# Kernel optimization log

Measured on AMD Instinct MI355X. Metric: run time of the kernel, lower is better.

## Reference

```python
import jax, jax.numpy as jnp
import numpy as np

B, S, D, H = 1, 4096, 768, 12
HID = 3072
HD = D // H  # 64
EPS = 1e-5


def _layer_norm(x, w, b):
    mean = jnp.mean(x, axis=-1, keepdims=True)
    var = jnp.mean(jnp.square(x - mean), axis=-1, keepdims=True)  # unbiased=False
    return w * ((x - mean) / jnp.sqrt(var + EPS)) + b


def setup_inputs() -> dict:
    key = jax.random.key(0)
    ks = jax.random.split(key, 8)
    s_d = 1.0 / np.sqrt(D)
    s_h = 1.0 / np.sqrt(HID)
    return {
        "x": jax.random.normal(ks[0], (B, S, D), dtype=jnp.float32),
        "Wqkv": jax.random.normal(ks[1], (D, 3 * D), dtype=jnp.float32) * s_d,
        "bqkv": jnp.zeros((3 * D,), dtype=jnp.float32),
        "Wo": jax.random.normal(ks[2], (D, D), dtype=jnp.float32) * s_d,
        "bo": jnp.zeros((D,), dtype=jnp.float32),
        "ln1_w": jnp.ones((D,), dtype=jnp.float32),
        "ln1_b": jnp.zeros((D,), dtype=jnp.float32),
        "W1": jax.random.normal(ks[3], (D, HID), dtype=jnp.float32) * s_d,
        "b1": jnp.zeros((HID,), dtype=jnp.float32),
        "W2": jax.random.normal(ks[4], (HID, D), dtype=jnp.float32) * s_h,
        "b2": jnp.zeros((D,), dtype=jnp.float32),
        "ln2_w": jnp.ones((D,), dtype=jnp.float32),
        "ln2_b": jnp.zeros((D,), dtype=jnp.float32),
    }


def reference(x, Wqkv, bqkv, Wo, bo, ln1_w, ln1_b, W1, b1, W2, b2, ln2_w, ln2_b):
    b, s, d = x.shape
    # --- multi-head self-attention (naive: full [B,H,S,S] scores) ---
    qkv = x @ Wqkv + bqkv                              # [B,S,3D]
    q, k, v = jnp.split(qkv, 3, axis=-1)
    split = lambda t: t.reshape(b, s, H, HD).transpose(0, 2, 1, 3)  # [B,H,S,hd]
    q, k, v = split(q), split(k), split(v)
    scores = jnp.einsum("bhqd,bhkd->bhqk", q, k) / jnp.sqrt(jnp.float32(HD))
    attn_w = jax.nn.softmax(scores, axis=-1)           # [B,H,S,S]
    h = jnp.einsum("bhqk,bhkd->bhqd", attn_w, v)
    h = h.transpose(0, 2, 1, 3).reshape(b, s, d)       # merge heads
    attn_out = h @ Wo + bo
    # --- post-norm residual 1 ---
    x1 = _layer_norm(x + attn_out, ln1_w, ln1_b)
    # --- FFN ---
    ff = jax.nn.gelu(x1 @ W1 + b1, approximate=False) @ W2 + b2
    # --- post-norm residual 2 ---
    return _layer_norm(x1 + ff, ln2_w, ln2_b)
```

## Files before the change

kernel.cpp:

```cpp
#include <hip/hip_runtime.h>
#include <hip/hip_bf16.h>

typedef __attribute__((ext_vector_type(8))) short bf16x8;
typedef __attribute__((ext_vector_type(4))) short short4v;
typedef __attribute__((ext_vector_type(4))) float f32x4;
typedef __attribute__((ext_vector_type(16))) float f32x16;
typedef __attribute__((ext_vector_type(4))) unsigned int uint4v;

__device__ inline unsigned short f2b(float f){
  unsigned int u = __float_as_uint(f);
  unsigned int r = (u + 0x7fffu + ((u >> 16) & 1u)) >> 16;
  return (unsigned short)r;
}
__device__ inline float b2f(unsigned short u){
  return __uint_as_float(((unsigned int)u) << 16);
}
__device__ inline unsigned int pk_fast(float lo, float hi){
  return ((__float_as_uint(hi) + 0x8000u) & 0xffff0000u)
       | ((__float_as_uint(lo) + 0x8000u) >> 16);
}
__device__ inline float pair_sum(float x){
  return x + __shfl_xor(x, 32);
}

__global__ __launch_bounds__(256) void prep_kernel(
    const float* __restrict__ Wqkv, short* __restrict__ WqkvT,
    const float* __restrict__ Wo,   short* __restrict__ WoT,
    const float* __restrict__ W1,   short* __restrict__ W1T,
    const float* __restrict__ W2,   short* __restrict__ W2T,
    const float* __restrict__ x,    short* __restrict__ xb){
  __shared__ float tile[32][33];
  const int b = blockIdx.x;
  const float* A; short* AT; int R, C, bx, by;
  if (b < 1728){ A=Wqkv; AT=WqkvT; R=768;  C=2304; bx=b%72;        by=b/72; }
  else if (b < 2304){ int c=b-1728; A=Wo; AT=WoT; R=768;  C=768;  bx=c%24; by=c/24; }
  else if (b < 4608){ int c=b-2304; A=W1; AT=W1T; R=768;  C=3072; bx=c%96; by=c/96; }
  else if (b < 6912){ int c=b-4608; A=W2; AT=W2T; R=3072; C=768;  bx=c%24; by=c/24; }
  else {
    int i = (b - 6912)*256 + threadIdx.x;
    float4 v = reinterpret_cast<const float4*>(x)[i];
    short4v o;
    o[0] = (short)f2b(v.x); o[1] = (short)f2b(v.y);
    o[2] = (short)f2b(v.z); o[3] = (short)f2b(v.w);
    reinterpret_cast<short4v*>(xb)[i] = o;
    return;
  }
  const int tx = threadIdx.x & 31, ty = threadIdx.x >> 5;
  const int c0 = bx*32, r0 = by*32;
  #pragma unroll
  for (int i = 0; i < 4; i++)
    tile[ty + i*8][tx] = A[(size_t)(r0 + ty + i*8)*C + c0 + tx];
  __syncthreads();
  #pragma unroll
  for (int i = 0; i < 4; i++){
    int c = c0 + ty + i*8, r = r0 + tx;
    AT[(size_t)c*R + r] = (short)f2b(tile[tx][ty + i*8]);
  }
}

template<int OUTMODE, int RESID, int GELU>
__global__ __launch_bounds__(256) void gemm_kernel(
    const short* __restrict__ A, const short* __restrict__ BT,
    const float* __restrict__ bias, const float* __restrict__ resid,
    float* __restrict__ outF, short* __restrict__ outB, short* __restrict__ outB2,
    short* __restrict__ outB3,
    int M, int N, int K)
{
  __shared__ short As[2][128*32];
  __shared__ short Bs[2][128*32];
  const int nwg = gridDim.x;
  const int wg = (blockIdx.x & 7) * (nwg >> 3) + (blockIdx.x >> 3);
  const int gx = N >> 7;
  const int bx = wg % gx, by = wg / gx;
  const int m0 = by * 128, n0 = bx * 128;

  const int lane = threadIdx.x & 63, wid = threadIdx.x >> 6;
  const int l15 = lane & 15, l4 = lane >> 4;
  const int wr = wid >> 1, wc = wid & 1;

  f32x4 acc[4][4];
  #pragma unroll
  for (int i = 0; i < 4; i++)
    #pragma unroll
    for (int j = 0; j < 4; j++) acc[i][j] = (f32x4){0.f,0.f,0.f,0.f};

  const int arow = wid*16 + (lane >> 2);
  const int sswz = (((lane & 3) ^ ((lane >> 3) & 3))) * 8;
  const short* Ag = A  + (size_t)(m0 + arow)*K + sswz;
  const short* Bg = BT + (size_t)(n0 + arow)*K + sswz;

  const int NT = K >> 5;

  auto STAGE = [&](int buf, int k0){
    #pragma unroll
    for (int p = 0; p < 2; p++){
      __builtin_amdgcn_global_load_lds(
          (const __attribute__((address_space(1))) void*)(Ag + (size_t)p*64*K + k0),
          (__attribute__((address_space(3))) void*)(&As[buf][(p*64 + wid*16)*32]), 16, 0, 0);
      __builtin_amdgcn_global_load_lds(
          (const __attribute__((address_space(1))) void*)(Bg + (size_t)p*64*K + k0),
          (__attribute__((address_space(3))) void*)(&Bs[buf][(p*64 + wid*16)*32]), 16, 0, 0);
    }
  };

  STAGE(0, 0);
  __syncthreads();

  const int rchunk = (l15 >> 1) & 3;
  for (int t = 0; t < NT; t++){
    if (t + 1 < NT) STAGE((t + 1) & 1, (t + 1) << 5);
    const short* as = &As[t & 1][0];
    const short* bs = &Bs[t & 1][0];
    bf16x8 av[4], bv[4];
    #pragma unroll
    for (int i = 0; i < 4; i++)
      av[i] = *(const bf16x8*)(as + (wr*64 + i*16 + l15)*32 + ((l4 ^ rchunk) * 8));
    #pragma unroll
    for (int i = 0; i < 4; i++)
      bv[i] = *(const bf16x8*)(bs + (wc*64 + i*16 + l15)*32 + ((l4 ^ rchunk) * 8));
    #pragma unroll
    for (int i = 0; i < 4; i++)
      #pragma unroll
      for (int j = 0; j < 4; j++)
        acc[i][j] = __builtin_amdgcn_mfma_f32_16x16x32_bf16(av[i], bv[j], acc[i][j], 0, 0, 0);
    __syncthreads();
  }

  if constexpr (OUTMODE == 2){
    #pragma unroll
    for (int i = 0; i < 4; i++){
      const int row0 = m0 + wr*64 + i*16 + l4*4;
      const size_t rQK = (size_t)(row0>>5)*2048 + (size_t)(row0&31)*8;
      const size_t rV  = (size_t)(row0>>5)*2048 + (size_t)((row0>>4)&1)*1024
                       + (size_t)((row0>>3)&1)*256 + (size_t)(row0&7);
      #pragma unroll
      for (int j = 0; j < 4; j++){
        const int col = n0 + wc*64 + j*16 + l15;
        const float bval = bias[col];
        const float v0 = acc[i][j][0] + bval, v1 = acc[i][j][1] + bval;
        const float v2 = acc[i][j][2] + bval, v3 = acc[i][j][3] + bval;
        if (col < 1536){
          const int c2 = (col < 768) ? col : (col - 768);
          short* dst = (col < 768) ? outB : outB2;
          const int head = c2 >> 6, dh = c2 & 63;
          const size_t base = (size_t)head*262144 + (size_t)(dh>>4)*512
                            + (size_t)((dh>>3)&1)*256 + (size_t)(dh&7) + rQK;
          dst[base]      = (short)f2b(v0);
          dst[base + 8]  = (short)f2b(v1);
          dst[base + 16] = (short)f2b(v2);
          dst[base + 24] = (short)f2b(v3);
        } else {
          const int c2 = col - 1536;
          const int head = c2 >> 6, dh = c2 & 63;
          const size_t base = (size_t)head*262144 + (size_t)(dh>>5)*512
                            + (size_t)(dh&31)*8 + rV;
          short4v sv;
          sv[0] = (short)f2b(v0); sv[1] = (short)f2b(v1);
          sv[2] = (short)f2b(v2); sv[3] = (short)f2b(v3);
          *(short4v*)(outB3 + base) = sv;
        }
      }
    }
  } else {
    #pragma unroll
    for (int i = 0; i < 4; i++){
      const int row0 = m0 + wr*64 + i*16 + l4*4;
      #pragma unroll
      for (int j = 0; j < 4; j++){
        const int col = n0 + wc*64 + j*16 + l15;
        const float bval = bias[col];
        #pragma unroll
        for (int jj = 0; jj < 4; jj++){
          const int row = row0 + jj;
          float v = acc[i][j][jj] + bval;
          if constexpr (RESID) v += resid[(size_t)row*N + col];
          if constexpr (GELU)  v = 0.5f * v * (1.f + erff(v * 0.70710678118654752f));
          if constexpr (OUTMODE == 0){
            outF[(size_t)row*N + col] = v;
          } else {
            outB[(size_t)row*N + col] = (short)f2b(v);
          }
        }
      }
    }
  }
}

__global__ __launch_bounds__(256) void attn5_kernel(
    const short* __restrict__ Qf, const short* __restrict__ Kf,
    const short* __restrict__ Vf, short* __restrict__ hout){
  __shared__ float Ols[4][32][33];
  __shared__ float Lls[4][32];
  const int head = blockIdx.y;
  const int qt = blockIdx.x;
  const int lane = threadIdx.x & 63, w = threadIdx.x >> 6;
  const int l31 = lane & 31, hi = lane >> 5;

  bf16x8 qf0, qf1, qf2, qf3;
  {
    const short* qp = Qf + (size_t)(head*128 + qt)*2048 + lane*8;
    const float SC = 0.125f * 1.44269504088896341f;
    bf16x8 tq[4];
    #pragma unroll
    for (int kd = 0; kd < 4; kd++){
      bf16x8 t = *(const bf16x8*)(qp + kd*512);
      #pragma unroll
      for (int i = 0; i < 8; i++)
        t[i] = (short)f2b(b2f((unsigned short)t[i]) * SC);
      tq[kd] = t;
    }
    qf0 = tq[0]; qf1 = tq[1]; qf2 = tq[2]; qf3 = tq[3];
  }

  float l_run = 0.f;
  f32x16 o0, o1;
  #pragma unroll
  for (int r = 0; r < 16; r++){ o0[r] = 0.f; o1[r] = 0.f; }

  const short* kp0 = Kf + (size_t)(head*128 + w*32)*2048 + lane*8;
  const short* vp0 = Vf + (size_t)(head*128 + w*32)*2048 + lane*8;

  auto PROC = [&](bf16x8 k0, bf16x8 k1, bf16x8 k2, bf16x8 k3, int t){
    const short* vp = vp0 + t*2048;
    bf16x8 v00 = *(const bf16x8*)(vp);
    bf16x8 v01 = *(const bf16x8*)(vp + 512);
    bf16x8 v10 = *(const bf16x8*)(vp + 1024);
    bf16x8 v11 = *(const bf16x8*)(vp + 1536);

    f32x16 s;
    #pragma unroll
    for (int r = 0; r < 16; r++) s[r] = 0.f;
    s = __builtin_amdgcn_mfma_f32_32x32x16_bf16(k0, qf0, s, 0, 0, 0);
    s = __builtin_amdgcn_mfma_f32_32x32x16_bf16(k1, qf1, s, 0, 0, 0);
    s = __builtin_amdgcn_mfma_f32_32x32x16_bf16(k2, qf2, s, 0, 0, 0);
    s = __builtin_amdgcn_mfma_f32_32x32x16_bf16(k3, qf3, s, 0, 0, 0);

    #pragma unroll
    for (int r = 0; r < 16; r++) s[r] = __builtin_amdgcn_exp2f(s[r]);
    float c0s = (s[0]+s[1]) + (s[2]+s[3]);
    float c1s = (s[4]+s[5]) + (s[6]+s[7]);
    float c2s = (s[8]+s[9]) + (s[10]+s[11]);
    float c3s = (s[12]+s[13]) + (s[14]+s[15]);
    l_run += pair_sum((c0s + c1s) + (c2s + c3s));

    unsigned int c01 = pk_fast(s[0],  s[1]),  c23 = pk_fast(s[2],  s[3]);
    unsigned int c45 = pk_fast(s[4],  s[5]),  c67 = pk_fast(s[6],  s[7]);
    unsigned int c89 = pk_fast(s[8],  s[9]),  cab = pk_fast(s[10], s[11]);
    unsigned int ccd = pk_fast(s[12], s[13]), cef = pk_fast(s[14], s[15]);
    unsigned int x01 = (unsigned int)__shfl_xor((int)c01, 32);
    unsigned int x23 = (unsigned int)__shfl_xor((int)c23, 32);
    unsigned int x45 = (unsigned int)__shfl_xor((int)c45, 32);
    unsigned int x67 = (unsigned int)__shfl_xor((int)c67, 32);
    unsigned int x89 = (unsigned int)__shfl_xor((int)c89, 32);
    unsigned int xab = (unsigned int)__shfl_xor((int)cab, 32);
    unsigned int xcd = (unsigned int)__shfl_xor((int)ccd, 32);
    unsigned int xef = (unsigned int)__shfl_xor((int)cef, 32);
    uint4v u0 = { hi ? x45 : c01, hi ? x67 : c23, hi ? c45 : x01, hi ? c67 : x23 };
    uint4v u1 = { hi ? xcd : c89, hi ? xef : cab, hi ? ccd : x89, hi ? cef : xab };
    bf16x8 pb0 = __builtin_bit_cast(bf16x8, u0);
    bf16x8 pb1 = __builtin_bit_cast(bf16x8, u1);

    o0 = __builtin_amdgcn_mfma_f32_32x32x16_bf16(v00, pb0, o0, 0, 0, 0);
    o0 = __builtin_amdgcn_mfma_f32_32x32x16_bf16(v10, pb1, o0, 0, 0, 0);
    o1 = __builtin_amdgcn_mfma_f32_32x32x16_bf16(v01, pb0, o1, 0, 0, 0);
    o1 = __builtin_amdgcn_mfma_f32_32x32x16_bf16(v11, pb1, o1, 0, 0, 0);
  };

  bf16x8 kA0 = *(const bf16x8*)(kp0);
  bf16x8 kA1 = *(const bf16x8*)(kp0 + 512);
  bf16x8 kA2 = *(const bf16x8*)(kp0 + 1024);
  bf16x8 kA3 = *(const bf16x8*)(kp0 + 1536);
  for (int t = 0; t < 32; t += 2){
    const short* kpB = kp0 + (t+1)*2048;
    bf16x8 kB0 = *(const bf16x8*)(kpB);
    bf16x8 kB1 = *(const bf16x8*)(kpB + 512);
    bf16x8 kB2 = *(const bf16x8*)(kpB + 1024);
    bf16x8 kB3 = *(const bf16x8*)(kpB + 1536);
    PROC(kA0, kA1, kA2, kA3, t);
    const short* kpA = kp0 + ((t+2 < 32) ? (t+2) : 31)*2048;
    kA0 = *(const bf16x8*)(kpA);
    kA1 = *(const bf16x8*)(kpA + 512);
    kA2 = *(const bf16x8*)(kpA + 1024);
    kA3 = *(const bf16x8*)(kpA + 1536);
    PROC(kB0, kB1, kB2, kB3, t+1);
  }

  if (hi == 0) Lls[w][l31] = l_run;
  #pragma unroll
  for (int r = 0; r < 16; r++){
    int d = (r & 3) + 8*(r >> 2) + 4*hi;
    Ols[w][l31][d] = o0[r];
  }
  __syncthreads();
  const int t = threadIdx.x;
  const int q = t >> 2, dc = (t & 3) * 8;
  float inv;
  if (t < 128){
    float l = Lls[0][q] + Lls[1][q] + Lls[2][q] + Lls[3][q];
    inv = 1.f / l;
    bf16x8 res;
    #pragma unroll
    for (int j = 0; j < 8; j++){
      float o = Ols[0][q][dc+j] + Ols[1][q][dc+j]
              + Ols[2][q][dc+j] + Ols[3][q][dc+j];
      res[j] = (short)f2b(o * inv);
    }
    *(bf16x8*)(hout + (size_t)(qt*32 + q)*768 + head*64 + dc) = res;
  }
  __syncthreads();
  #pragma unroll
  for (int r = 0; r < 16; r++){
    int d = (r & 3) + 8*(r >> 2) + 4*hi;
    Ols[w][l31][d] = o1[r];
  }
  __syncthreads();
  if (t < 128){
    bf16x8 res;
    #pragma unroll
    for (int j = 0; j < 8; j++){
      float o = Ols[0][q][dc+j] + Ols[1][q][dc+j]
              + Ols[2][q][dc+j] + Ols[3][q][dc+j];
      res[j] = (short)f2b(o * inv);
    }
    *(bf16x8*)(hout + (size_t)(qt*32 + q)*768 + head*64 + 32 + dc) = res;
  }
}

template<int WRITE_BF16>
__global__ __launch_bounds__(256) void ln_kernel(
    const float* __restrict__ in, const float* __restrict__ g, const float* __restrict__ b,
    float* __restrict__ outF, short* __restrict__ outB){
  const int row = blockIdx.x;
  const float* x = in + (size_t)row * 768;
  const int t = threadIdx.x;
  float v[3];
  #pragma unroll
  for (int i = 0; i < 3; i++) v[i] = x[t + i*256];
  float s  = v[0] + v[1] + v[2];
  float s2 = v[0]*v[0] + v[1]*v[1] + v[2]*v[2];
  #pragma unroll
  for (int off = 1; off < 64; off <<= 1){
    s  += __shfl_xor(s,  off);
    s2 += __shfl_xor(s2, off);
  }
  __shared__ float red[8];
  if ((t & 63) == 0){ red[t >> 6] = s; red[4 + (t >> 6)] = s2; }
  __syncthreads();
  s  = red[0] + red[1] + red[2] + red[3];
  s2 = red[4] + red[5] + red[6] + red[7];
  const float mean = s * (1.f/768.f);
  const float rstd = rsqrtf(s2*(1.f/768.f) - mean*mean + 1e-5f);
  #pragma unroll
  for (int i = 0; i < 3; i++){
    int c = t + i*256;
    float y = g[c] * ((v[i] - mean) * rstd) + b[c];
    outF[(size_t)row*768 + c] = y;
    if constexpr (WRITE_BF16) outB[(size_t)row*768 + c] = (short)f2b(y);
  }
}

extern "C" void kernel_launch(void* const* d_in, const int* in_sizes, int n_in,
                              void* d_out, int out_size, void* d_ws, size_t ws_size,
                              hipStream_t stream){
  const float* x    = (const float*)d_in[0];
  const float* Wqkv = (const float*)d_in[1];
  const float* bqkv = (const float*)d_in[2];
  const float* Wo   = (const float*)d_in[3];
  const float* bo   = (const float*)d_in[4];
  const float* ln1w = (const float*)d_in[5];
  const float* ln1b = (const float*)d_in[6];
  const float* W1   = (const float*)d_in[7];
  const float* b1   = (const float*)d_in[8];
  const float* W2   = (const float*)d_in[9];
  const float* b2   = (const float*)d_in[10];
  const float* ln2w = (const float*)d_in[11];
  const float* ln2b = (const float*)d_in[12];
  float* out = (float*)d_out;

  char* ws = (char*)d_ws;
  short* WqkvT = (short*)(ws + 0);
  short* WoT   = (short*)(ws + 3538944);
  short* W1T   = (short*)(ws + 4718592);
  short* W2T   = (short*)(ws + 9437184);
  short* xb    = (short*)(ws + 14155776);
  short* Qfb   = (short*)(ws + 20447232);
  short* Kfb   = (short*)(ws + 26738688);
  short* Vfb   = (short*)(ws + 33030144);
  short* hb    = (short*)(ws + 39321600);
  float* res1  = (float*)(ws + 45613056);
  float* x1f   = (float*)(ws + 58195968);
  short* x1b   = (short*)(ws + 70778880);
  short* h1b   = (short*)(ws + 77070336);
  float* y2 = res1;

  dim3 blk(256);
  prep_kernel<<<dim3(9984), blk, 0, stream>>>(
      Wqkv, WqkvT, Wo, WoT, W1, W1T, W2, W2T, x, xb);

  gemm_kernel<2,0,0><<<dim3(576), blk, 0, stream>>>(
      xb, WqkvT, bqkv, nullptr, nullptr, Qfb, Kfb, Vfb, 4096, 2304, 768);
  attn5_kernel<<<dim3(128, 12), blk, 0, stream>>>(Qfb, Kfb, Vfb, hb);
  gemm_kernel<0,1,0><<<dim3(192), blk, 0, stream>>>(
      hb, WoT, bo, x, res1, nullptr, nullptr, nullptr, 4096, 768, 768);
  ln_kernel<1><<<dim3(4096), blk, 0, stream>>>(res1, ln1w, ln1b, x1f, x1b);
  gemm_kernel<1,0,1><<<dim3(768), blk, 0, stream>>>(
      x1b, W1T, b1, nullptr, nullptr, h1b, nullptr, nullptr, 4096, 3072, 768);
  gemm_kernel<0,1,0><<<dim3(192), blk, 0, stream>>>(
      h1b, W2T, b2, x1f, y2, nullptr, nullptr, nullptr, 4096, 768, 3072);
  ln_kernel<0><<<dim3(4096), blk, 0, stream>>>(y2, ln2w, ln2b, out, nullptr);
}
```

Before: 248.2 us.

## Triple-buffer GEMM LDS staging and pack two query tiles per attention block

The GEMM main loop moves from double to triple buffering. It issues loads two tiles ahead and replaces the per-iteration __syncthreads with an explicit vmcnt wait plus a single barrier, so global-to-LDS copies overlap more MFMA work. The attention kernel now runs 512 threads per block, covering two 32-row query tiles per block with doubled LDS reduction buffers. This halves the block count and lets the two tiles share a block. The cost is more LDS per block, which may lower occupancy, and the hand-written vmcnt counting must stay correct.

```diff
diff --git a/kernel.cpp b/kernel.cpp
--- a/kernel.cpp
+++ b/kernel.cpp
@@ -66,8 +66,8 @@
     short* __restrict__ outB3,
     int M, int N, int K)
 {
-  __shared__ short As[2][128*32];
-  __shared__ short Bs[2][128*32];
+  __shared__ short As[3][128*32];
+  __shared__ short Bs[3][128*32];
   const int nwg = gridDim.x;
   const int wg = (blockIdx.x & 7) * (nwg >> 3) + (blockIdx.x >> 3);
   const int gx = N >> 7;
@@ -104,13 +104,17 @@
   };
 
   STAGE(0, 0);
-  __syncthreads();
+  STAGE(1, 32);
 
   const int rchunk = (l15 >> 1) & 3;
+  int cur = 0;
   for (int t = 0; t < NT; t++){
-    if (t + 1 < NT) STAGE((t + 1) & 1, (t + 1) << 5);
-    const short* as = &As[t & 1][0];
-    const short* bs = &Bs[t & 1][0];
+    if (t + 1 < NT) asm volatile("s_waitcnt vmcnt(4)" ::: "memory");
+    else            asm volatile("s_waitcnt vmcnt(0)" ::: "memory");
+    __builtin_amdgcn_s_barrier();
+    __builtin_amdgcn_sched_barrier(0);
+    const short* as = &As[cur][0];
+    const short* bs = &Bs[cur][0];
     bf16x8 av[4], bv[4];
     #pragma unroll
     for (int i = 0; i < 4; i++)
@@ -123,7 +127,11 @@
       #pragma unroll
       for (int j = 0; j < 4; j++)
         acc[i][j] = __builtin_amdgcn_mfma_f32_16x16x32_bf16(av[i], bv[j], acc[i][j], 0, 0, 0);
-    __syncthreads();
+    if (t + 2 < NT){
+      int s2 = cur + 2; if (s2 >= 3) s2 -= 3;
+      STAGE(s2, (t + 2) << 5);
+    }
+    cur = (cur == 2) ? 0 : cur + 1;
   }
 
   if constexpr (OUTMODE == 2){
@@ -186,14 +194,17 @@
   }
 }
 
-__global__ __launch_bounds__(256) void attn5_kernel(
+__global__ __launch_bounds__(512) void attn6_kernel(
     const short* __restrict__ Qf, const short* __restrict__ Kf,
     const short* __restrict__ Vf, short* __restrict__ hout){
-  __shared__ float Ols[4][32][33];
-  __shared__ float Lls[4][32];
+  __shared__ float Ols[2][4][32][33];
+  __shared__ float Lls[2][4][32];
   const int head = blockIdx.y;
-  const int qt = blockIdx.x;
-  const int lane = threadIdx.x & 63, w = threadIdx.x >> 6;
+  const int qt2 = blockIdx.x;
+  const int tid = threadIdx.x;
+  const int lane = tid & 63, w8 = tid >> 6;
+  const int set = w8 >> 2, w = w8 & 3;
+  const int qt = qt2*2 + set;
   const int l31 = lane & 31, hi = lane >> 5;
 
   bf16x8 qf0, qf1, qf2, qf3;
@@ -285,44 +296,45 @@
     PROC(kB0, kB1, kB2, kB3, t+1);
   }
 
-  if (hi == 0) Lls[w][l31] = l_run;
+  if (hi == 0) Lls[set][w][l31] = l_run;
   #pragma unroll
   for (int r = 0; r < 16; r++){
     int d = (r & 3) + 8*(r >> 2) + 4*hi;
-    Ols[w][l31][d] = o0[r];
+    Ols[set][w][l31][d] = o0[r];
   }
   __syncthreads();
-  const int t = threadIdx.x;
-  const int q = t >> 2, dc = (t & 3) * 8;
+  const int mset = tid >> 8, mt = tid & 255;
+  const int q = mt >> 2, dc = (mt & 3) * 8;
+  const int qrow = qt2*64 + mset*32 + q;
   float inv;
-  if (t < 128){
-    float l = Lls[0][q] + Lls[1][q] + Lls[2][q] + Lls[3][q];
+  if (mt < 128){
+    float l = Lls[mset][0][q] + Lls[mset][1][q] + Lls[mset][2][q] + Lls[mset][3][q];
     inv = 1.f / l;
     bf16x8 res;
     #pragma unroll
     for (int j = 0; j < 8; j++){
-      float o = Ols[0][q][dc+j] + Ols[1][q][dc+j]
-              + Ols[2][q][dc+j] + Ols[3][q][dc+j];
+      float o = Ols[mset][0][q][dc+j] + Ols[mset][1][q][dc+j]
+              + Ols[mset][2][q][dc+j] + Ols[mset][3][q][dc+j];
       res[j] = (short)f2b(o * inv);
     }
-    *(bf16x8*)(hout + (size_t)(qt*32 + q)*768 + head*64 + dc) = res;
+    *(bf16x8*)(hout + (size_t)qrow*768 + head*64 + dc) = res;
   }
   __syncthreads();
   #pragma unroll
   for (int r = 0; r < 16; r++){
     int d = (r & 3) + 8*(r >> 2) + 4*hi;
-    Ols[w][l31][d] = o1[r];
+    Ols[set][w][l31][d] = o1[r];
   }
   __syncthreads();
-  if (t < 128){
+  if (mt < 128){
     bf16x8 res;
     #pragma unroll
     for (int j = 0; j < 8; j++){
-      float o = Ols[0][q][dc+j] + Ols[1][q][dc+j]
-              + Ols[2][q][dc+j] + Ols[3][q][dc+j];
+      float o = Ols[mset][0][q][dc+j] + Ols[mset][1][q][dc+j]
+              + Ols[mset][2][q][dc+j] + Ols[mset][3][q][dc+j];
       res[j] = (short)f2b(o * inv);
     }
-    *(bf16x8*)(hout + (size_t)(qt*32 + q)*768 + head*64 + 32 + dc) = res;
+    *(bf16x8*)(hout + (size_t)qrow*768 + head*64 + 32 + dc) = res;
   }
 }
 
@@ -399,7 +411,7 @@
 
   gemm_kernel<2,0,0><<<dim3(576), blk, 0, stream>>>(
       xb, WqkvT, bqkv, nullptr, nullptr, Qfb, Kfb, Vfb, 4096, 2304, 768);
-  attn5_kernel<<<dim3(128, 12), blk, 0, stream>>>(Qfb, Kfb, Vfb, hb);
+  attn6_kernel<<<dim3(64, 12), dim3(512), 0, stream>>>(Qfb, Kfb, Vfb, hb);
   gemm_kernel<0,1,0><<<dim3(192), blk, 0, stream>>>(
       hb, WoT, bo, x, res1, nullptr, nullptr, nullptr, 4096, 768, 768);
   ln_kernel<1><<<dim3(4096), blk, 0, stream>>>(res1, ln1w, ln1b, x1f, x1b);
```

After: 275.9 us. 1.11x slower.
